# Optimization experiments

Measured on AMD Instinct MI355X. Metric: run time of the kernel, lower is better.

## Reference

```python
import jax, jax.numpy as jnp
import numpy as np

BETA = 0.25
EPS = 1e-10


def setup_inputs() -> dict:
    key = jax.random.key(0)
    k1, k2 = jax.random.split(key)
    x = jax.random.normal(k1, (32, 64, 64, 64), dtype=jnp.float32)  # [B, C=embed_dim, H, W]
    embeddings = jax.random.normal(k2, (64, 512), dtype=jnp.float32)  # [embed_dim, K]
    return {"x": x, "embeddings": embeddings}


def reference(x, embeddings):
    B, C, H, W = x.shape
    K = embeddings.shape[1]
    sg = jax.lax.stop_gradient

    z_e = jnp.transpose(x, (0, 2, 3, 1))          # [B, H, W, C]
    z_flat = z_e.reshape(-1, C)                    # [N, C]

    # Squared L2 distances to codebook: ||z||^2 + ||e||^2 - 2 z.e
    dists = (
        jnp.sum(z_flat * z_flat, axis=1, keepdims=True)
        + jnp.sum(embeddings * embeddings, axis=0)
        - 2.0 * (z_flat @ embeddings)
    )                                              # [N, K]
    idx = jnp.argmin(dists, axis=1)                # [N]

    # Direct gather instead of one-hot matmul (same math)
    quantized = embeddings.T[idx].reshape(z_e.shape)  # [B, H, W, C]

    e_latent_loss = jnp.mean((sg(quantized) - z_e) ** 2)
    q_latent_loss = jnp.mean((quantized - sg(z_e)) ** 2)
    loss = q_latent_loss + BETA * e_latent_loss

    # Straight-through estimator
    quantized_st = z_e + sg(quantized - z_e)

    # Perplexity via codebook usage histogram (== mean of one-hot encodings)
    N = idx.shape[0]
    counts = jnp.zeros((K,), dtype=jnp.float32).at[idx].add(1.0)
    avg_probs = counts / N
    perplexity = jnp.exp(-jnp.sum(avg_probs * jnp.log(avg_probs + EPS)))

    quantized_out = jnp.transpose(quantized_st, (0, 3, 1, 2))  # [B, C, H, W]
    encoding_indices = idx.reshape(B, H, W)
    return loss, quantized_out, perplexity, encoding_indices
```

## Files before the change

### kernel.cpp

```cpp
#include <hip/hip_runtime.h>


#define B_ 32
#define C_ 64
#define HW_ 4096
#define K_ 512
#define N_ (B_ * HW_)
#define NC_ ((long long)N_ * C_)
#define ROWS_ 128
#define NBLK_ (N_ / ROWS_)
#define HBLK_ 64

typedef __attribute__((ext_vector_type(8))) short short8;
typedef __attribute__((ext_vector_type(4))) float float4_t;


__device__ __forceinline__ unsigned short f2bf(float f) {
    unsigned u = __float_as_uint(f);
    u += 0x7fffu + ((u >> 16) & 1u);
    return (unsigned short)(u >> 16);
}
__device__ __forceinline__ float bf2f(unsigned short h) {
    return __uint_as_float(((unsigned)h) << 16);
}
__device__ __forceinline__ int offA(int r, int c) {
    return ((r >> 4) << 10) + ((c >> 3) << 7) + ((r & 15) << 3) + (c & 7);
}
__device__ __forceinline__ void merge2(float& m1, int& i1, float& m2,
                                       float om1, int oi1, float om2) {
    if (om1 < m1) { m2 = fminf(m1, om2); m1 = om1; i1 = oi1; }
    else          { m2 = fminf(m2, om1); }
}

__global__ __launch_bounds__(512) void vq_init(const float* __restrict__ emb,
                                               float* __restrict__ snmax_p,
                                               float* __restrict__ en,
                                               float* __restrict__ embT32,
                                               unsigned short* __restrict__ fBhi,
                                               unsigned short* __restrict__ fBlo) {
    __shared__ float smax[8];
    int k = threadIdx.x;
    if (blockIdx.x < 64) {
        int c = blockIdx.x;
        float e = emb[c * K_ + k];
        embT32[k * C_ + c] = e;
        float s = -2.0f * e;
        unsigned short hi = f2bf(s);
        unsigned short lo = f2bf(s - bf2f(hi));
        int kk   = c >> 5;
        int lane = (((c & 31) >> 3) << 4) + (k & 15);
        int fb   = ((k >> 5) << 2) + (((k >> 4) & 1) << 1) + kk;
        int off  = (fb << 9) + (lane << 3) + (c & 7);
        fBhi[off] = hi;
        fBlo[off] = lo;
    } else {
        float s = 0.f;
#pragma unroll
        for (int c = 0; c < C_; ++c) {
            float e = emb[c * K_ + k];
            s += e * e;
        }
        en[k] = s;
        float m = s;
#pragma unroll
        for (int off = 32; off > 0; off >>= 1)
            m = fmaxf(m, __shfl_down(m, off, 64));
        if ((k & 63) == 0) smax[k >> 6] = m;
        __syncthreads();
        if (k == 0) {
            float mm = smax[0];
#pragma unroll
            for (int w2 = 1; w2 < 8; ++w2) mm = fmaxf(mm, smax[w2]);
            *snmax_p = 4.0f * mm;
        }
    }
}

__global__ __launch_bounds__(256, 3) void vq_main(const float* __restrict__ x,
                                                  const float* __restrict__ en_g,
                                                  const float* __restrict__ embT32,
                                                  const unsigned short* __restrict__ fBhi,
                                                  const unsigned short* __restrict__ fBlo,
                                                  const float* __restrict__ snmax_p,
                                                  float* __restrict__ out_q,
                                                  float* __restrict__ out_idx,
                                                  double* __restrict__ ssepart) {
    __shared__ unsigned short Ahi[ROWS_ * C_];
    __shared__ unsigned short Alo[ROWS_ * C_];
    __shared__ float znp[2 * ROWS_];
    __shared__ float sEn[K_];
    __shared__ int   biarr[ROWS_];
    __shared__ int   flaglist[ROWS_];
    __shared__ float wsse[4];
    __shared__ int   nflag;

    const int t   = threadIdx.x;
    const int n0  = blockIdx.x * ROWS_;
    const int b   = n0 >> 12;
    const int hw0 = n0 & 4095;
    const float* xbase = x + ((size_t)b << 18) + hw0;

    if (t == 0) nflag = 0;
    sEn[t]       = en_g[t];
    sEn[256 + t] = en_g[256 + t];

    float znacc = 0.f;
#pragma unroll 8
    for (int i = 0; i < 32; ++i) {
        int id = (i << 8) + t;
        int c = id >> 7;
        int r = id & 127;
        float v = xbase[((size_t)c << 12) + r];
        znacc += v * v;
        unsigned short hi = f2bf(v);
        unsigned short lo = f2bf(v - bf2f(hi));
        int o = offA(r, c);
        Ahi[o] = hi;
        Alo[o] = lo;
    }
    znp[((t >> 7) << 7) + (t & 127)] = znacc;
    __syncthreads();

    const int lane = t & 63;
    const int w    = t >> 6;
    const int ln15 = lane & 15;
    const int quad = lane >> 4;
    const float snm = *snmax_p;

    short8 ah[2][2], al[2][2];
#pragma unroll
    for (int rtl = 0; rtl < 2; ++rtl) {
        int ab = (((2 * w) + rtl) << 10) + (quad << 7) + (ln15 << 3);
        ah[rtl][0] = *(const short8*)(Ahi + ab);
        ah[rtl][1] = *(const short8*)(Ahi + ab + 512);
        al[rtl][0] = *(const short8*)(Alo + ab);
        al[rtl][1] = *(const short8*)(Alo + ab + 512);
    }

    float m1[2][4], m2[2][4];
    int   i1[2][4];
#pragma unroll
    for (int rtl = 0; rtl < 2; ++rtl)
#pragma unroll
        for (int reg = 0; reg < 4; ++reg) {
            m1[rtl][reg] = 3.4e38f; m2[rtl][reg] = 3.4e38f; i1[rtl][reg] = 0;
        }

    for (int p = 0; p < 16; ++p) {
#pragma unroll
        for (int ct = 0; ct < 2; ++ct) {
            const unsigned short* fh = fBhi + ((((p << 2) + (ct << 1)) << 9) + (lane << 3));
            const unsigned short* fl = fBlo + ((((p << 2) + (ct << 1)) << 9) + (lane << 3));
            short8 bh0 = *(const short8*)(fh);
            short8 bh1 = *(const short8*)(fh + 512);
            short8 bl0 = *(const short8*)(fl);
            short8 bl1 = *(const short8*)(fl + 512);
            float env = sEn[(p << 5) + (ct << 4) + ln15];
            int   idx = (p << 5) + (ct << 4) + ln15;
#pragma unroll
            for (int rtl = 0; rtl < 2; ++rtl) {
                float4_t a = {0.f, 0.f, 0.f, 0.f};
                a = __builtin_amdgcn_mfma_f32_16x16x32_bf16(ah[rtl][0], bh0, a, 0, 0, 0);
                a = __builtin_amdgcn_mfma_f32_16x16x32_bf16(ah[rtl][1], bh1, a, 0, 0, 0);
                a = __builtin_amdgcn_mfma_f32_16x16x32_bf16(ah[rtl][0], bl0, a, 0, 0, 0);
                a = __builtin_amdgcn_mfma_f32_16x16x32_bf16(ah[rtl][1], bl1, a, 0, 0, 0);
                a = __builtin_amdgcn_mfma_f32_16x16x32_bf16(al[rtl][0], bh0, a, 0, 0, 0);
                a = __builtin_amdgcn_mfma_f32_16x16x32_bf16(al[rtl][1], bh1, a, 0, 0, 0);
#pragma unroll
                for (int reg = 0; reg < 4; ++reg) {
                    float v = a[reg] + env;
                    if (v < m1[rtl][reg]) {
                        m2[rtl][reg] = m1[rtl][reg]; m1[rtl][reg] = v; i1[rtl][reg] = idx;
                    } else {
                        m2[rtl][reg] = fminf(m2[rtl][reg], v);
                    }
                }
            }
        }
    }

#pragma unroll
    for (int rtl = 0; rtl < 2; ++rtl)
#pragma unroll
        for (int reg = 0; reg < 4; ++reg) {
            float a1 = m1[rtl][reg], a2 = m2[rtl][reg];
            int   ai = i1[rtl][reg];
#pragma unroll
            for (int s = 1; s < 16; s <<= 1) {
                float o1 = __shfl_xor(a1, s, 16);
                int   oi = __shfl_xor(ai, s, 16);
                float o2 = __shfl_xor(a2, s, 16);
                merge2(a1, ai, a2, o1, oi, o2);
            }
            if (ln15 == 0) {
                int row = (((2 * w) + rtl) << 4) + (quad << 2) + reg;
                float znr = znp[row] + znp[128 + row];
                float W = 1.4e-4f * __builtin_sqrtf(znr * snm) + 1e-3f;
                biarr[row] = ai;
                if (a2 > a1 + W) {
                    out_idx[n0 + row] = (float)ai;
                } else {
                    int pos = atomicAdd(&nflag, 1);
                    flaglist[pos] = row;
                }
            }
        }
    __syncthreads();

    int nf = nflag;
    for (int f = w; f < nf; f += 4) {
        int r = flaglist[f];
        float zl = xbase[((size_t)lane << 12) + r];
        float d[8];
#pragma unroll
        for (int j = 0; j < 8; ++j) d[j] = 0.f;
        for (int c4 = 0; c4 < 16; ++c4) {
            float z0 = __shfl(zl, (c4 << 2) + 0, 64);
            float z1 = __shfl(zl, (c4 << 2) + 1, 64);
            float z2 = __shfl(zl, (c4 << 2) + 2, 64);
            float z3 = __shfl(zl, (c4 << 2) + 3, 64);
#pragma unroll
            for (int j = 0; j < 8; ++j) {
                float4 e = *(const float4*)(embT32 + ((((lane << 3) + j) << 6) + (c4 << 2)));
                d[j] = fmaf(z0, e.x, d[j]);
                d[j] = fmaf(z1, e.y, d[j]);
                d[j] = fmaf(z2, e.z, d[j]);
                d[j] = fmaf(z3, e.w, d[j]);
            }
        }
        float znr = znp[r] + znp[128 + r];
        float best = 3.4e38f;
        int   bidx = 0;
#pragma unroll
        for (int j = 0; j < 8; ++j) {
            int k = (lane << 3) + j;
            float dist = (znr + sEn[k]) - 2.f * d[j];
            if (dist < best) { best = dist; bidx = k; }
        }
#pragma unroll
        for (int off = 32; off > 0; off >>= 1) {
            float ov = __shfl_down(best, off, 64);
            int   oi = __shfl_down(bidx, off, 64);
            if (ov < best || (ov == best && oi < bidx)) { best = ov; bidx = oi; }
        }
        if (lane == 0) {
            biarr[r] = bidx;
            out_idx[n0 + r] = (float)bidx;
        }
    }
    __syncthreads();

    float sacc = 0.f;
#pragma unroll
    for (int i = 0; i < 2; ++i) {
        int id2 = (i << 8) + t;
        int r  = id2 & 127;
        int p2 = id2 >> 7;
        int code = biarr[r];
        const float* ebase = embT32 + ((code << 6) + (p2 << 4));
        float* qb = out_q + ((size_t)b << 18) + hw0 + r;
#pragma unroll
        for (int j = 0; j < 4; ++j) {
            float4 q4 = *(const float4*)(ebase + (j << 2));
            int c = (p2 << 4) + (j << 2);
            int o = offA(r, c);
            ushort4 h4 = *(const ushort4*)(Ahi + o);
            ushort4 l4 = *(const ushort4*)(Alo + o);
            float z0 = bf2f(h4.x) + bf2f(l4.x);
            float z1 = bf2f(h4.y) + bf2f(l4.y);
            float z2 = bf2f(h4.z) + bf2f(l4.z);
            float z3 = bf2f(h4.w) + bf2f(l4.w);
            float d0 = q4.x - z0, d1 = q4.y - z1, d2 = q4.z - z2, d3 = q4.w - z3;
            sacc += d0 * d0 + d1 * d1 + d2 * d2 + d3 * d3;
            qb[(size_t)(c + 0) << 12] = q4.x;
            qb[(size_t)(c + 1) << 12] = q4.y;
            qb[(size_t)(c + 2) << 12] = q4.z;
            qb[(size_t)(c + 3) << 12] = q4.w;
        }
    }
#pragma unroll
    for (int off = 32; off > 0; off >>= 1)
        sacc += __shfl_down(sacc, off, 64);
    if (lane == 0) wsse[w] = sacc;
    __syncthreads();
    if (t == 0)
        ssepart[blockIdx.x] = (double)wsse[0] + (double)wsse[1]
                            + (double)wsse[2] + (double)wsse[3];
}

__global__ __launch_bounds__(256) void vq_hist(const float* __restrict__ out_idx,
                                               int* __restrict__ histpart) {
    __shared__ int h[K_];
    int t = threadIdx.x;
    h[t] = 0; h[t + 256] = 0;
    __syncthreads();
    const float* ip = out_idx + blockIdx.x * (N_ / HBLK_);
#pragma unroll
    for (int i = 0; i < (N_ / HBLK_) / 256; ++i) {
        int k = (int)ip[(i << 8) + t];
        atomicAdd(&h[k], 1);
    }
    __syncthreads();
    histpart[blockIdx.x * K_ + t]       = h[t];
    histpart[blockIdx.x * K_ + 256 + t] = h[t + 256];
}

__global__ __launch_bounds__(512) void vq_final(const int* __restrict__ histpart,
                                                const double* __restrict__ ssepart,
                                                float* __restrict__ out_loss,
                                                float* __restrict__ out_perp) {
    __shared__ float  wsf[8];
    __shared__ double wsd[8];
    int t = threadIdx.x;
    int hsum = 0;
#pragma unroll 8
    for (int b = 0; b < HBLK_; ++b)
        hsum += histpart[b * K_ + t];
    float p = (float)hsum / (float)N_;
    float s = p * logf(p + 1e-10f);
    double d = ssepart[t] + ssepart[t + 512];
#pragma unroll
    for (int off = 32; off > 0; off >>= 1) {
        s += __shfl_down(s, off, 64);
        d += __shfl_down(d, off, 64);
    }
    if ((t & 63) == 0) { wsf[t >> 6] = s; wsd[t >> 6] = d; }
    __syncthreads();
    if (t == 0) {
        float  S = 0.f;
        double D = 0.0;
#pragma unroll
        for (int w = 0; w < 8; ++w) { S += wsf[w]; D += wsd[w]; }
        *out_perp = expf(-S);
        *out_loss = (float)(1.25 * D / (double)NC_);
    }
}

extern "C" void kernel_launch(void* const* d_in, const int* in_sizes, int n_in,
                              void* d_out, int out_size, void* d_ws, size_t ws_size,
                              hipStream_t stream) {
    const float* x   = (const float*)d_in[0];
    const float* emb = (const float*)d_in[1];

    float* out      = (float*)d_out;
    float* out_loss = out;
    float* out_q    = out + 1;
    float* out_perp = out + 1 + (size_t)N_ * C_;
    float* out_idx  = out + 2 + (size_t)N_ * C_;

    char* ws = (char*)d_ws;
    float*          snmax_p  = (float*)(ws + 56);
    float*          en       = (float*)(ws + 2112);
    float*          embT32   = (float*)(ws + 4160);
    unsigned short* fBhi     = (unsigned short*)(ws + 135232);
    unsigned short* fBlo     = (unsigned short*)(ws + 200768);
    double*         ssepart  = (double*)(ws + 266304);
    int*            histpart = (int*)(ws + 274496);

    vq_init<<<65, 512, 0, stream>>>(emb, snmax_p, en, embT32, fBhi, fBlo);
    vq_main<<<NBLK_, 256, 0, stream>>>(x, en, embT32, fBhi, fBlo, snmax_p,
                                       out_q, out_idx, ssepart);
    vq_hist<<<HBLK_, 256, 0, stream>>>(out_idx, histpart);
    vq_final<<<1, 512, 0, stream>>>(histpart, ssepart, out_loss, out_perp);
}
```

Measured before the change: 161.2 us.

## Halve rows per block, reuse one LDS tile for hi/lo splits

Rows per block drop from 128 to 64, so each wave handles one 16-row tile instead of two. The hi and lo bf16 halves now share a single LDS buffer in two phases, which cuts shared memory and drops the launch-bounds occupancy hint. The MFMA chain is split into two independent accumulators to shorten the dependency chain. The epilogue rebuilds z from register fragments instead of LDS, and histpart now reuses the fB workspace region. The trade-off is twice as many blocks, and each block reloads the codebook fragments from global memory, so that traffic doubles.

```diff
diff --git a/kernel.cpp b/kernel.cpp
--- a/kernel.cpp
+++ b/kernel.cpp
@@ -7,7 +7,7 @@
 #define K_ 512
 #define N_ (B_ * HW_)
 #define NC_ ((long long)N_ * C_)
-#define ROWS_ 128
+#define ROWS_ 64
 #define NBLK_ (N_ / ROWS_)
 #define HBLK_ 64
 
@@ -76,19 +76,18 @@
     }
 }
 
-__global__ __launch_bounds__(256, 3) void vq_main(const float* __restrict__ x,
-                                                  const float* __restrict__ en_g,
-                                                  const float* __restrict__ embT32,
-                                                  const unsigned short* __restrict__ fBhi,
-                                                  const unsigned short* __restrict__ fBlo,
-                                                  const float* __restrict__ snmax_p,
-                                                  float* __restrict__ out_q,
-                                                  float* __restrict__ out_idx,
-                                                  double* __restrict__ ssepart) {
-    __shared__ unsigned short Ahi[ROWS_ * C_];
-    __shared__ unsigned short Alo[ROWS_ * C_];
-    __shared__ float znp[2 * ROWS_];
+__global__ __launch_bounds__(256) void vq_argmin(const float* __restrict__ x,
+                                                 const float* __restrict__ en_g,
+                                                 const float* __restrict__ embT32,
+                                                 const unsigned short* __restrict__ fBhi,
+                                                 const unsigned short* __restrict__ fBlo,
+                                                 const float* __restrict__ snmax_p,
+                                                 float* __restrict__ out_q,
+                                                 float* __restrict__ out_idx,
+                                                 double* __restrict__ ssepart) {
+    __shared__ unsigned short Ast[ROWS_ * C_];
     __shared__ float sEn[K_];
+    __shared__ float znp[4 * ROWS_];
     __shared__ int   biarr[ROWS_];
     __shared__ int   flaglist[ROWS_];
     __shared__ float wsse[4];
@@ -104,21 +103,19 @@
     sEn[t]       = en_g[t];
     sEn[256 + t] = en_g[256 + t];
 
+    float v[16];
     float znacc = 0.f;
-#pragma unroll 8
-    for (int i = 0; i < 32; ++i) {
+#pragma unroll
+    for (int i = 0; i < 16; ++i) {
         int id = (i << 8) + t;
-        int c = id >> 7;
-        int r = id & 127;
-        float v = xbase[((size_t)c << 12) + r];
-        znacc += v * v;
-        unsigned short hi = f2bf(v);
-        unsigned short lo = f2bf(v - bf2f(hi));
-        int o = offA(r, c);
-        Ahi[o] = hi;
-        Alo[o] = lo;
-    }
-    znp[((t >> 7) << 7) + (t & 127)] = znacc;
+        int c = id >> 6;
+        int r = id & 63;
+        float val = xbase[((size_t)c << 12) + r];
+        v[i] = val;
+        znacc += val * val;
+        Ast[offA(r, c)] = f2bf(val);
+    }
+    znp[((t >> 6) << 6) + (t & 63)] = znacc;
     __syncthreads();
 
     const int lane = t & 63;
@@ -127,84 +124,85 @@
     const int quad = lane >> 4;
     const float snm = *snmax_p;
 
-    short8 ah[2][2], al[2][2];
-#pragma unroll
-    for (int rtl = 0; rtl < 2; ++rtl) {
-        int ab = (((2 * w) + rtl) << 10) + (quad << 7) + (ln15 << 3);
-        ah[rtl][0] = *(const short8*)(Ahi + ab);
-        ah[rtl][1] = *(const short8*)(Ahi + ab + 512);
-        al[rtl][0] = *(const short8*)(Alo + ab);
-        al[rtl][1] = *(const short8*)(Alo + ab + 512);
-    }
-
-    float m1[2][4], m2[2][4];
-    int   i1[2][4];
-#pragma unroll
-    for (int rtl = 0; rtl < 2; ++rtl)
-#pragma unroll
-        for (int reg = 0; reg < 4; ++reg) {
-            m1[rtl][reg] = 3.4e38f; m2[rtl][reg] = 3.4e38f; i1[rtl][reg] = 0;
-        }
+    const int ab = (w << 10) + (quad << 7) + (ln15 << 3);
+    short8 ah0 = *(const short8*)(Ast + ab);
+    short8 ah1 = *(const short8*)(Ast + ab + 512);
+    __syncthreads();
+
+#pragma unroll
+    for (int i = 0; i < 16; ++i) {
+        int id = (i << 8) + t;
+        int c = id >> 6;
+        int r = id & 63;
+        float val = v[i];
+        unsigned short hi = f2bf(val);
+        Ast[offA(r, c)] = f2bf(val - bf2f(hi));
+    }
+    __syncthreads();
+    short8 al0 = *(const short8*)(Ast + ab);
+    short8 al1 = *(const short8*)(Ast + ab + 512);
+
+    float m1[4], m2[4];
+    int   i1[4];
+#pragma unroll
+    for (int reg = 0; reg < 4; ++reg) {
+        m1[reg] = 3.4e38f; m2[reg] = 3.4e38f; i1[reg] = 0;
+    }
 
     for (int p = 0; p < 16; ++p) {
 #pragma unroll
         for (int ct = 0; ct < 2; ++ct) {
-            const unsigned short* fh = fBhi + ((((p << 2) + (ct << 1)) << 9) + (lane << 3));
-            const unsigned short* fl = fBlo + ((((p << 2) + (ct << 1)) << 9) + (lane << 3));
-            short8 bh0 = *(const short8*)(fh);
-            short8 bh1 = *(const short8*)(fh + 512);
-            short8 bl0 = *(const short8*)(fl);
-            short8 bl1 = *(const short8*)(fl + 512);
+            const int fbase = ((((p << 2) + (ct << 1)) << 9) + (lane << 3));
+            short8 bh0 = *(const short8*)(fBhi + fbase);
+            short8 bh1 = *(const short8*)(fBhi + fbase + 512);
+            short8 bl0 = *(const short8*)(fBlo + fbase);
+            short8 bl1 = *(const short8*)(fBlo + fbase + 512);
             float env = sEn[(p << 5) + (ct << 4) + ln15];
             int   idx = (p << 5) + (ct << 4) + ln15;
-#pragma unroll
-            for (int rtl = 0; rtl < 2; ++rtl) {
-                float4_t a = {0.f, 0.f, 0.f, 0.f};
-                a = __builtin_amdgcn_mfma_f32_16x16x32_bf16(ah[rtl][0], bh0, a, 0, 0, 0);
-                a = __builtin_amdgcn_mfma_f32_16x16x32_bf16(ah[rtl][1], bh1, a, 0, 0, 0);
-                a = __builtin_amdgcn_mfma_f32_16x16x32_bf16(ah[rtl][0], bl0, a, 0, 0, 0);
-                a = __builtin_amdgcn_mfma_f32_16x16x32_bf16(ah[rtl][1], bl1, a, 0, 0, 0);
-                a = __builtin_amdgcn_mfma_f32_16x16x32_bf16(al[rtl][0], bh0, a, 0, 0, 0);
-                a = __builtin_amdgcn_mfma_f32_16x16x32_bf16(al[rtl][1], bh1, a, 0, 0, 0);
-#pragma unroll
-                for (int reg = 0; reg < 4; ++reg) {
-                    float v = a[reg] + env;
-                    if (v < m1[rtl][reg]) {
-                        m2[rtl][reg] = m1[rtl][reg]; m1[rtl][reg] = v; i1[rtl][reg] = idx;
-                    } else {
-                        m2[rtl][reg] = fminf(m2[rtl][reg], v);
-                    }
+            float4_t a0 = {0.f, 0.f, 0.f, 0.f};
+            float4_t a1 = {0.f, 0.f, 0.f, 0.f};
+            a0 = __builtin_amdgcn_mfma_f32_16x16x32_bf16(al0, bh0, a0, 0, 0, 0);
+            a1 = __builtin_amdgcn_mfma_f32_16x16x32_bf16(al1, bh1, a1, 0, 0, 0);
+            a0 = __builtin_amdgcn_mfma_f32_16x16x32_bf16(ah0, bl0, a0, 0, 0, 0);
+            a1 = __builtin_amdgcn_mfma_f32_16x16x32_bf16(ah1, bl1, a1, 0, 0, 0);
+            a0 = __builtin_amdgcn_mfma_f32_16x16x32_bf16(ah0, bh0, a0, 0, 0, 0);
+            a1 = __builtin_amdgcn_mfma_f32_16x16x32_bf16(ah1, bh1, a1, 0, 0, 0);
+#pragma unroll
+            for (int reg = 0; reg < 4; ++reg) {
+                float vv = (a0[reg] + a1[reg]) + env;
+                if (vv < m1[reg]) {
+                    m2[reg] = m1[reg]; m1[reg] = vv; i1[reg] = idx;
+                } else {
+                    m2[reg] = fminf(m2[reg], vv);
                 }
             }
         }
     }
 
 #pragma unroll
-    for (int rtl = 0; rtl < 2; ++rtl)
-#pragma unroll
-        for (int reg = 0; reg < 4; ++reg) {
-            float a1 = m1[rtl][reg], a2 = m2[rtl][reg];
-            int   ai = i1[rtl][reg];
-#pragma unroll
-            for (int s = 1; s < 16; s <<= 1) {
-                float o1 = __shfl_xor(a1, s, 16);
-                int   oi = __shfl_xor(ai, s, 16);
-                float o2 = __shfl_xor(a2, s, 16);
-                merge2(a1, ai, a2, o1, oi, o2);
+    for (int reg = 0; reg < 4; ++reg) {
+        float a1v = m1[reg], a2v = m2[reg];
+        int   ai  = i1[reg];
+#pragma unroll
+        for (int s = 1; s < 16; s <<= 1) {
+            float o1 = __shfl_xor(a1v, s, 16);
+            int   oi = __shfl_xor(ai, s, 16);
+            float o2 = __shfl_xor(a2v, s, 16);
+            merge2(a1v, ai, a2v, o1, oi, o2);
+        }
+        if (ln15 == 0) {
+            int row = (w << 4) + (quad << 2) + reg;
+            float znr = znp[row] + znp[64 + row] + znp[128 + row] + znp[192 + row];
+            float W = 1.4e-4f * __builtin_sqrtf(znr * snm) + 1e-3f;
+            biarr[row] = ai;
+            if (a2v > a1v + W) {
+                out_idx[n0 + row] = (float)ai;
+            } else {
+                int pos = atomicAdd(&nflag, 1);
+                flaglist[pos] = row;
             }
-            if (ln15 == 0) {
-                int row = (((2 * w) + rtl) << 4) + (quad << 2) + reg;
-                float znr = znp[row] + znp[128 + row];
-                float W = 1.4e-4f * __builtin_sqrtf(znr * snm) + 1e-3f;
-                biarr[row] = ai;
-                if (a2 > a1 + W) {
-                    out_idx[n0 + row] = (float)ai;
-                } else {
-                    int pos = atomicAdd(&nflag, 1);
-                    flaglist[pos] = row;
-                }
-            }
-        }
+        }
+    }
     __syncthreads();
 
     int nf = nflag;
@@ -221,14 +219,14 @@
             float z3 = __shfl(zl, (c4 << 2) + 3, 64);
 #pragma unroll
             for (int j = 0; j < 8; ++j) {
-                float4 e = *(const float4*)(embT32 + ((((lane << 3) + j) << 6) + (c4 << 2)));
-                d[j] = fmaf(z0, e.x, d[j]);
-                d[j] = fmaf(z1, e.y, d[j]);
-                d[j] = fmaf(z2, e.z, d[j]);
-                d[j] = fmaf(z3, e.w, d[j]);
+                float4_t e = *(const float4_t*)(embT32 + ((((lane << 3) + j) << 6) + (c4 << 2)));
+                d[j] = fmaf(z0, e[0], d[j]);
+                d[j] = fmaf(z1, e[1], d[j]);
+                d[j] = fmaf(z2, e[2], d[j]);
+                d[j] = fmaf(z3, e[3], d[j]);
             }
         }
-        float znr = znp[r] + znp[128 + r];
+        float znr = znp[r] + znp[64 + r] + znp[128 + r] + znp[192 + r];
         float best = 3.4e38f;
         int   bidx = 0;
 #pragma unroll
@@ -250,33 +248,31 @@
     }
     __syncthreads();
 
+    const int myrow = (w << 4) + ln15;
+    const int code  = biarr[myrow];
+    const float* eb = embT32 + (code << 6) + (quad << 3);
+    float4_t e0 = *(const float4_t*)(eb);
+    float4_t e1 = *(const float4_t*)(eb + 4);
+    float4_t e2 = *(const float4_t*)(eb + 32);
+    float4_t e3 = *(const float4_t*)(eb + 36);
+    float* qrow = out_q + ((size_t)b << 18) + hw0 + myrow;
     float sacc = 0.f;
 #pragma unroll
-    for (int i = 0; i < 2; ++i) {
-        int id2 = (i << 8) + t;
-        int r  = id2 & 127;
-        int p2 = id2 >> 7;
-        int code = biarr[r];
-        const float* ebase = embT32 + ((code << 6) + (p2 << 4));
-        float* qb = out_q + ((size_t)b << 18) + hw0 + r;
-#pragma unroll
-        for (int j = 0; j < 4; ++j) {
-            float4 q4 = *(const float4*)(ebase + (j << 2));
-            int c = (p2 << 4) + (j << 2);
-            int o = offA(r, c);
-            ushort4 h4 = *(const ushort4*)(Ahi + o);
-            ushort4 l4 = *(const ushort4*)(Alo + o);
-            float z0 = bf2f(h4.x) + bf2f(l4.x);
-            float z1 = bf2f(h4.y) + bf2f(l4.y);
-            float z2 = bf2f(h4.z) + bf2f(l4.z);
-            float z3 = bf2f(h4.w) + bf2f(l4.w);
-            float d0 = q4.x - z0, d1 = q4.y - z1, d2 = q4.z - z2, d3 = q4.w - z3;
-            sacc += d0 * d0 + d1 * d1 + d2 * d2 + d3 * d3;
-            qb[(size_t)(c + 0) << 12] = q4.x;
-            qb[(size_t)(c + 1) << 12] = q4.y;
-            qb[(size_t)(c + 2) << 12] = q4.z;
-            qb[(size_t)(c + 3) << 12] = q4.w;
-        }
+    for (int j = 0; j < 4; ++j) {
+        int c0 = (quad << 3) + j;
+        int c1 = (quad << 3) + 4 + j;
+        float zA = bf2f((unsigned short)ah0[j])     + bf2f((unsigned short)al0[j]);
+        float zB = bf2f((unsigned short)ah0[4 + j]) + bf2f((unsigned short)al0[4 + j]);
+        float dA = e0[j] - zA, dB = e1[j] - zB;
+        sacc += dA * dA + dB * dB;
+        qrow[(size_t)c0 << 12] = e0[j];
+        qrow[(size_t)c1 << 12] = e1[j];
+        float zC = bf2f((unsigned short)ah1[j])     + bf2f((unsigned short)al1[j]);
+        float zD = bf2f((unsigned short)ah1[4 + j]) + bf2f((unsigned short)al1[4 + j]);
+        float dC = e2[j] - zC, dD = e3[j] - zD;
+        sacc += dC * dC + dD * dD;
+        qrow[(size_t)(32 + c0) << 12] = e2[j];
+        qrow[(size_t)(32 + c1) << 12] = e3[j];
     }
 #pragma unroll
     for (int off = 32; off > 0; off >>= 1)
@@ -318,7 +314,7 @@
         hsum += histpart[b * K_ + t];
     float p = (float)hsum / (float)N_;
     float s = p * logf(p + 1e-10f);
-    double d = ssepart[t] + ssepart[t + 512];
+    double d = ssepart[t] + ssepart[t + 512] + ssepart[t + 1024] + ssepart[t + 1536];
 #pragma unroll
     for (int off = 32; off > 0; off >>= 1) {
         s += __shfl_down(s, off, 64);
@@ -354,12 +350,12 @@
     float*          embT32   = (float*)(ws + 4160);
     unsigned short* fBhi     = (unsigned short*)(ws + 135232);
     unsigned short* fBlo     = (unsigned short*)(ws + 200768);
+    int*            histpart = (int*)(ws + 135232);
     double*         ssepart  = (double*)(ws + 266304);
-    int*            histpart = (int*)(ws + 274496);
 
     vq_init<<<65, 512, 0, stream>>>(emb, snmax_p, en, embT32, fBhi, fBlo);
-    vq_main<<<NBLK_, 256, 0, stream>>>(x, en, embT32, fBhi, fBlo, snmax_p,
-                                       out_q, out_idx, ssepart);
+    vq_argmin<<<NBLK_, 256, 0, stream>>>(x, en, embT32, fBhi, fBlo, snmax_p,
+                                         out_q, out_idx, ssepart);
     vq_hist<<<HBLK_, 256, 0, stream>>>(out_idx, histpart);
     vq_final<<<1, 512, 0, stream>>>(histpart, ssepart, out_loss, out_perp);
 }
```

New measurement: 154.6 us. 1.04x faster.
